# Kernel optimization log

Hardware: AMD Instinct MI355X
Metric: run time of the kernel (lower is better)

The kernel has to match this reference:

```python
import jax, jax.numpy as jnp
import numpy as np

NUM_SAMPLES = 128
NEAR = 0.1
FAR = 2.0
B = 4
NUM_RAYS = 65536


def setup_inputs() -> dict:
    key = jax.random.key(0)
    k1, k2 = jax.random.split(key)
    rgb = jax.random.uniform(k1, (B, NUM_RAYS, NUM_SAMPLES, 3), dtype=jnp.float32)
    density = jax.random.uniform(k2, (B, NUM_RAYS, NUM_SAMPLES), dtype=jnp.float32)
    return {"rgb": rgb, "density": density}


def reference(rgb, density):
    # t_vals: deterministic linspace (eval mode, no stratified noise)
    t_vals = jnp.linspace(NEAR, FAR, NUM_SAMPLES, dtype=jnp.float32)  # [S]
    t_vals = jnp.broadcast_to(t_vals, (B, NUM_RAYS, NUM_SAMPLES))

    # deltas between consecutive samples; last delta is huge (1e10)
    deltas = t_vals[:, :, 1:] - t_vals[:, :, :-1]
    last_delta = jnp.full((B, NUM_RAYS, 1), 1e10, dtype=jnp.float32)
    deltas = jnp.concatenate([deltas, last_delta], axis=2)  # [B,R,S]

    alpha = 1.0 - jnp.exp(-density * deltas)  # [B,R,S]

    # exclusive cumulative product transmittance
    trans_inner = jnp.cumprod(1.0 - alpha + 1e-10, axis=-1)  # [B,R,S]
    ones = jnp.ones((B, NUM_RAYS, 1), dtype=jnp.float32)
    transmittance = jnp.concatenate([ones, trans_inner], axis=-1)[:, :, :-1]  # [B,R,S]

    weights = alpha * transmittance  # [B,R,S]
    rendered_colors = jnp.sum(weights[..., None] * rgb, axis=-2)  # [B,R,3]
    return rendered_colors
```

## Files before the change

### kernel.cpp

```cpp
#include <hip/hip_runtime.h>


#define NSAMP 128
typedef float f32x4 __attribute__((ext_vector_type(4)));

__global__ __launch_bounds__(256) void VolumetricRayMarcher_kernel(
    const float* __restrict__ rgb,
    const float* __restrict__ density,
    float* __restrict__ out,
    int n_rays) {
    const int lane = threadIdx.x & 63;
    const int h    = lane >> 5;
    const int l    = lane & 31;
    const int wave = threadIdx.x >> 6;
    const int ray  = blockIdx.x * 8 + wave * 2 + h;
    if (ray >= n_rays) return;

    const float DELTA = 1.9f / 127.0f;

    const f32x4 d4 = ((const f32x4*)(density + (size_t)ray * NSAMP))[l];
    const f32x4* rg = (const f32x4*)(rgb + (size_t)ray * (NSAMP * 3)) + (size_t)l * 3;
    const f32x4 a = rg[0];
    const f32x4 b = rg[1];
    const f32x4 c = rg[2];

    const float dl3 = (l == 31) ? 1e10f : DELTA;
    const float al0 = 1.0f - __expf(-d4.x * DELTA);
    const float al1 = 1.0f - __expf(-d4.y * DELTA);
    const float al2 = 1.0f - __expf(-d4.z * DELTA);
    const float al3 = 1.0f - __expf(-d4.w * dl3);
    const float f0 = 1.0f - al0 + 1e-10f;
    const float f1 = 1.0f - al1 + 1e-10f;
    const float f2 = 1.0f - al2 + 1e-10f;
    const float f3 = 1.0f - al3 + 1e-10f;

    float p = (f0 * f1) * (f2 * f3);
    #pragma unroll
    for (int off = 1; off < 32; off <<= 1) {
        float o = __shfl_up(p, off, 32);
        if (l >= off) p *= o;
    }
    float excl = __shfl_up(p, 1, 32);
    if (l == 0) excl = 1.0f;

    float t = excl;
    const float w0 = al0 * t; t *= f0;
    const float w1 = al1 * t; t *= f1;
    const float w2 = al2 * t; t *= f2;
    const float w3 = al3 * t;

    float acc0 = w0 * a.x + w1 * a.w + w2 * b.z + w3 * c.y;
    float acc1 = w0 * a.y + w1 * b.x + w2 * b.w + w3 * c.z;
    float acc2 = w0 * a.z + w1 * b.y + w2 * c.x + w3 * c.w;

    #pragma unroll
    for (int off = 16; off > 0; off >>= 1) {
        acc0 += __shfl_xor(acc0, off, 32);
        acc1 += __shfl_xor(acc1, off, 32);
        acc2 += __shfl_xor(acc2, off, 32);
    }

    if (l == 0) {
        float* o = out + (size_t)ray * 3;
        o[0] = acc0;
        o[1] = acc1;
        o[2] = acc2;
    }
}

extern "C" void kernel_launch(void* const* d_in, const int* in_sizes, int n_in,
                              void* d_out, int out_size, void* d_ws, size_t ws_size,
                              hipStream_t stream) {
    const float* rgb     = (const float*)d_in[0];
    const float* density = (const float*)d_in[1];
    float* out = (float*)d_out;

    const int n_rays = in_sizes[1] / NSAMP;
    const int blocks = (n_rays + 7) / 8;

    hipLaunchKernelGGL(VolumetricRayMarcher_kernel, dim3(blocks), dim3(256), 0, stream,
                       rgb, density, out, n_rays);
}
```

Measured before the change: 95.28 us.

## Use persistent grid-stride waves with software-prefetched next ray pair

Replaces the one-pair-per-wave launch with a persistent grid capped at 2048 blocks, where each wave loops over ray pairs. Inside the loop it issues the next pair's density and rgb loads before computing the current pair, overlapping memory latency with the scan and reduction. This cuts block launch overhead and aims to keep more loads in flight per wave. In exchange it uses more registers for the double-buffered data and lowers occupancy, which could reduce memory-level parallelism on a bandwidth-bound kernel. An odd ray count would leave the last ray unprocessed.

```diff
diff --git a/kernel.cpp b/kernel.cpp
--- a/kernel.cpp
+++ b/kernel.cpp
@@ -8,63 +8,84 @@
     const float* __restrict__ rgb,
     const float* __restrict__ density,
     float* __restrict__ out,
-    int n_rays) {
+    int n_pairs) {
     const int lane = threadIdx.x & 63;
     const int h    = lane >> 5;
     const int l    = lane & 31;
-    const int wave = threadIdx.x >> 6;
-    const int ray  = blockIdx.x * 8 + wave * 2 + h;
-    if (ray >= n_rays) return;
+    const int wid  = (int)((blockIdx.x * blockDim.x + threadIdx.x) >> 6);
+    const int nw   = (int)((gridDim.x * blockDim.x) >> 6);
 
     const float DELTA = 1.9f / 127.0f;
+    const float dl3 = (l == 31) ? 1e10f : DELTA;
 
-    const f32x4 d4 = ((const f32x4*)(density + (size_t)ray * NSAMP))[l];
+    int pair = wid;
+    if (pair >= n_pairs) return;
+
+    int ray = pair * 2 + h;
+    f32x4 d4 = ((const f32x4*)(density + (size_t)ray * NSAMP))[l];
     const f32x4* rg = (const f32x4*)(rgb + (size_t)ray * (NSAMP * 3)) + (size_t)l * 3;
-    const f32x4 a = rg[0];
-    const f32x4 b = rg[1];
-    const f32x4 c = rg[2];
+    f32x4 a = rg[0];
+    f32x4 b = rg[1];
+    f32x4 c = rg[2];
 
-    const float dl3 = (l == 31) ? 1e10f : DELTA;
-    const float al0 = 1.0f - __expf(-d4.x * DELTA);
-    const float al1 = 1.0f - __expf(-d4.y * DELTA);
-    const float al2 = 1.0f - __expf(-d4.z * DELTA);
-    const float al3 = 1.0f - __expf(-d4.w * dl3);
-    const float f0 = 1.0f - al0 + 1e-10f;
-    const float f1 = 1.0f - al1 + 1e-10f;
-    const float f2 = 1.0f - al2 + 1e-10f;
-    const float f3 = 1.0f - al3 + 1e-10f;
+    while (true) {
+        const int npair = pair + nw;
+        const bool have_next = (npair < n_pairs);
+        f32x4 nd4 = d4, na = a, nb = b, nc = c;
+        if (have_next) {
+            const int nray = npair * 2 + h;
+            nd4 = ((const f32x4*)(density + (size_t)nray * NSAMP))[l];
+            const f32x4* nrg = (const f32x4*)(rgb + (size_t)nray * (NSAMP * 3)) + (size_t)l * 3;
+            na = nrg[0];
+            nb = nrg[1];
+            nc = nrg[2];
+        }
 
-    float p = (f0 * f1) * (f2 * f3);
-    #pragma unroll
-    for (int off = 1; off < 32; off <<= 1) {
-        float o = __shfl_up(p, off, 32);
-        if (l >= off) p *= o;
-    }
-    float excl = __shfl_up(p, 1, 32);
-    if (l == 0) excl = 1.0f;
+        const float al0 = 1.0f - __expf(-d4.x * DELTA);
+        const float al1 = 1.0f - __expf(-d4.y * DELTA);
+        const float al2 = 1.0f - __expf(-d4.z * DELTA);
+        const float al3 = 1.0f - __expf(-d4.w * dl3);
+        const float f0 = 1.0f - al0 + 1e-10f;
+        const float f1 = 1.0f - al1 + 1e-10f;
+        const float f2 = 1.0f - al2 + 1e-10f;
+        const float f3 = 1.0f - al3 + 1e-10f;
 
-    float t = excl;
-    const float w0 = al0 * t; t *= f0;
-    const float w1 = al1 * t; t *= f1;
-    const float w2 = al2 * t; t *= f2;
-    const float w3 = al3 * t;
+        float p = (f0 * f1) * (f2 * f3);
+        #pragma unroll
+        for (int off = 1; off < 32; off <<= 1) {
+            float o = __shfl_up(p, off, 32);
+            if (l >= off) p *= o;
+        }
+        float excl = __shfl_up(p, 1, 32);
+        if (l == 0) excl = 1.0f;
 
-    float acc0 = w0 * a.x + w1 * a.w + w2 * b.z + w3 * c.y;
-    float acc1 = w0 * a.y + w1 * b.x + w2 * b.w + w3 * c.z;
-    float acc2 = w0 * a.z + w1 * b.y + w2 * c.x + w3 * c.w;
+        float t = excl;
+        const float w0 = al0 * t; t *= f0;
+        const float w1 = al1 * t; t *= f1;
+        const float w2 = al2 * t; t *= f2;
+        const float w3 = al3 * t;
 
-    #pragma unroll
-    for (int off = 16; off > 0; off >>= 1) {
-        acc0 += __shfl_xor(acc0, off, 32);
-        acc1 += __shfl_xor(acc1, off, 32);
-        acc2 += __shfl_xor(acc2, off, 32);
-    }
+        float acc0 = w0 * a.x + w1 * a.w + w2 * b.z + w3 * c.y;
+        float acc1 = w0 * a.y + w1 * b.x + w2 * b.w + w3 * c.z;
+        float acc2 = w0 * a.z + w1 * b.y + w2 * c.x + w3 * c.w;
 
-    if (l == 0) {
-        float* o = out + (size_t)ray * 3;
-        o[0] = acc0;
-        o[1] = acc1;
-        o[2] = acc2;
+        #pragma unroll
+        for (int off = 16; off > 0; off >>= 1) {
+            acc0 += __shfl_xor(acc0, off, 32);
+            acc1 += __shfl_xor(acc1, off, 32);
+            acc2 += __shfl_xor(acc2, off, 32);
+        }
+
+        if (l == 0) {
+            float* o = out + (size_t)(pair * 2 + h) * 3;
+            o[0] = acc0;
+            o[1] = acc1;
+            o[2] = acc2;
+        }
+
+        if (!have_next) break;
+        pair = npair;
+        d4 = nd4; a = na; b = nb; c = nc;
     }
 }
 
@@ -75,9 +96,12 @@
     const float* density = (const float*)d_in[1];
     float* out = (float*)d_out;
 
-    const int n_rays = in_sizes[1] / NSAMP;
-    const int blocks = (n_rays + 7) / 8;
+    const int n_rays  = in_sizes[1] / NSAMP;
+    const int n_pairs = n_rays / 2;
+
+    int blocks = (n_pairs + 3) / 4;
+    if (blocks > 2048) blocks = 2048;
 
     hipLaunchKernelGGL(VolumetricRayMarcher_kernel, dim3(blocks), dim3(256), 0, stream,
-                       rgb, density, out, n_rays);
+                       rgb, density, out, n_pairs);
 }
```

Result: slower. 103.1 us (+8.2%).
